# Performance work log

Hardware: AMD Instinct MI355X
Metric: run time of the kernel (lower is better)

Reference implementation:

```python
import jax, jax.numpy as jnp
import numpy as np
import math

B, S, D, H = 4, 512, 768, 12
HD = D // H  # 64
NREL = 2 * 50 + 1  # 101


def setup_inputs() -> dict:
    key = jax.random.key(0)
    ks = jax.random.split(key, 16)
    sc = 0.02
    inp = {
        "query": jax.random.normal(ks[0], (B, S, D), jnp.float32),
        "key": jax.random.normal(ks[1], (B, S, D), jnp.float32),
        "value": jax.random.normal(ks[2], (B, S, D), jnp.float32),
        "mask": jax.random.randint(ks[3], (B, S), 0, 2, jnp.int32),
        "graph_arc": jax.random.randint(ks[4], (B, S, S), 0, NREL, jnp.int64),
        "Wq": jax.random.normal(ks[5], (D, D), jnp.float32) * sc,
        "bq": jnp.zeros((D,), jnp.float32),
        "Wk": jax.random.normal(ks[6], (D, D), jnp.float32) * sc,
        "bk": jnp.zeros((D,), jnp.float32),
        "Wv": jax.random.normal(ks[7], (D, D), jnp.float32) * sc,
        "bv": jnp.zeros((D,), jnp.float32),
        "Wo": jax.random.normal(ks[8], (D, D), jnp.float32) * sc,
        "bo": jnp.zeros((D,), jnp.float32),
        "Ek": jax.random.normal(ks[9], (NREL, HD), jnp.float32) * sc,  # dp_relation_k_g
        "Eq": jax.random.normal(ks[10], (NREL, HD), jnp.float32) * sc,  # dp_relation_q_g
        "Ev": jax.random.normal(ks[11], (NREL, HD), jnp.float32) * sc,  # dp_relation_v_g
    }
    return inp


def _shape(x):
    # (b, s, d) -> (b, h, s, hd)
    return x.reshape(B, S, H, HD).transpose(0, 2, 1, 3)


def reference(query, key, value, mask, graph_arc, Wq, bq, Wk, bk, Wv, bv, Wo, bo, Ek, Eq, Ev):
    q = _shape(query @ Wq.T + bq)   # (b, h, s, hd)
    k = _shape(key @ Wk.T + bk)
    v = _shape(value @ Wv.T + bv)

    scores = jnp.einsum('bhqe,bhke->bhqk', q, k)  # raw QK^T

    dp_k = Ek[graph_arc]  # (b, s, r, hd) relation key embeddings
    dp_q = Eq[graph_arc]  # (b, s, r, hd) relation query embeddings (use_two_attn)
    dp_v = Ev[graph_arc]  # (b, s, r, hd) relation value embeddings (not just_attn)

    key_dp = jnp.einsum('bhse,bsre->bhsr', q, dp_k)
    query_dp = jnp.einsum('bhse,bsre->bhsr', k, dp_q)
    scores = (scores + query_dp + key_dp) / math.sqrt(HD)

    neg_inf = jnp.float32(-jnp.inf)
    maskb = (mask == 0)[:, None, None, :]  # (b, 1, 1, k)
    scores = jnp.where(maskb, neg_inf, scores)
    weights = jax.nn.softmax(scores, axis=-1)  # (b, h, s, r)

    context = jnp.einsum('bhqk,bhke->bhqe', weights, v)
    # relative_matmul_dpv: (b,h,s,r) x (b,s,r,e) -> (b,h,s,e)
    context = context + jnp.einsum('bhsr,bsre->bhse', weights, dp_v)

    context = context.transpose(0, 2, 1, 3).reshape(B, S, D)  # unshape
    out = context @ Wo.T + bo
    return out
```

## Files before the change

### kernel.cpp

```cpp
#include <hip/hip_runtime.h>
#include <hip/hip_bf16.h>
#include <cfloat>
#include <cstdint>

#define Bb 4
#define Ss 512
#define Dd 768
#define Hh 12
#define HDd 64
#define NREL 101

typedef __attribute__((ext_vector_type(8))) short bfrag;
typedef __attribute__((ext_vector_type(4))) float f32x4;
typedef __attribute__((ext_vector_type(8))) unsigned short u16x8;

static __device__ __forceinline__ unsigned short f2bf(float x) {
  union { __hip_bfloat16 h; unsigned short u; } c;
  c.h = __float2bfloat16(x);
  return c.u;
}
static __device__ __forceinline__ float bf2f(unsigned short u) {
  return __uint_as_float(((unsigned int)u) << 16);
}
static __device__ __forceinline__ f32x4 mfma3(bfrag a, bfrag b, f32x4 c) {
  return __builtin_amdgcn_mfma_f32_16x16x32_bf16(a, b, c, 0, 0, 0);
}
static __device__ __forceinline__ void gload16(const void* g, void* l) {
  __builtin_amdgcn_global_load_lds((const __attribute__((address_space(1))) void*)g,
                                   (__attribute__((address_space(3))) void*)l, 16, 0, 0);
}

__global__ void detect_kernel(const int* __restrict__ g, int* __restrict__ flag) {
  __shared__ int anynz;
  if (threadIdx.x == 0) anynz = 0;
  __syncthreads();
  int acc = 0;
  for (int i = threadIdx.x; i < 4096; i += 256) acc |= g[2 * i + 1];
  if (acc != 0) atomicOr(&anynz, 1);
  __syncthreads();
  if (threadIdx.x == 0) *flag = (anynz == 0) ? 1 : 0;
}

__global__ __launch_bounds__(256) void relcvt_kernel(const int* __restrict__ g,
                                                     const int* __restrict__ flag,
                                                     unsigned char* __restrict__ rel8) {
  const int idx = blockIdx.x * 256 + threadIdx.x;
  uchar4 o;
  if (*flag) {
    const int4* p = (const int4*)g + (size_t)idx * 2;
    int4 a = p[0], b = p[1];
    o = make_uchar4((unsigned char)a.x, (unsigned char)a.z,
                    (unsigned char)b.x, (unsigned char)b.z);
  } else {
    int4 a = ((const int4*)g)[idx];
    o = make_uchar4((unsigned char)a.x, (unsigned char)a.y,
                    (unsigned char)a.z, (unsigned char)a.w);
  }
  ((uchar4*)rel8)[idx] = o;
}

__global__ __launch_bounds__(256) void epad_kernel(const float* __restrict__ Ek,
                                                   const float* __restrict__ Eq,
                                                   const float* __restrict__ Ev,
                                                   float* __restrict__ ekp,
                                                   float* __restrict__ eqp,
                                                   float* __restrict__ evtp) {
  const int i = blockIdx.x * 256 + threadIdx.x;
  if (i < 112 * 64) {
    const int rel = i >> 6;
    ekp[i] = (rel < NREL) ? Ek[i] : 0.f;
    eqp[i] = (rel < NREL) ? Eq[i] : 0.f;
  }
  if (i < 64 * 128) {
    const int d = i >> 7, g = i & 127;
    evtp[i] = (g < NREL) ? Ev[g * 64 + d] : 0.f;
  }
}

struct CvtJob { const float* src; unsigned short* hi; unsigned short* lo; int rowlen; int nslots; };
struct Cvt8 { CvtJob j[8]; };

__global__ __launch_bounds__(256) void convert_kernel(Cvt8 jobs) {
  CvtJob jb = jobs.j[blockIdx.z];
  int idx = blockIdx.x * 256 + threadIdx.x;
  if (idx >= jb.nslots) return;
  const int spr = jb.rowlen >> 3;
  const int row = idx / spr;
  const int srem = idx - row * spr;
  const int c = srem >> 3, s8 = srem & 7;
  const float4* s4 = (const float4*)(jb.src + (size_t)idx * 8);
  float4 v0 = s4[0], v1 = s4[1];
  float e[8] = {v0.x, v0.y, v0.z, v0.w, v1.x, v1.y, v1.z, v1.w};
  u16x8 H, L;
#pragma unroll
  for (int i = 0; i < 8; i++) {
    unsigned short h = f2bf(e[i]);
    H[i] = h;
    L[i] = f2bf(e[i] - bf2f(h));
  }
  size_t dst = (size_t)row * jb.rowlen + c * 64 + (size_t)((s8 ^ (row & 7)) * 8);
  *(u16x8*)(jb.hi + dst) = H;
  *(u16x8*)(jb.lo + dst) = L;
}

__global__ __launch_bounds__(256, 2) void gemm_mfma(
    const unsigned short* __restrict__ Xh0, const unsigned short* __restrict__ Xl0,
    const unsigned short* __restrict__ Xh1, const unsigned short* __restrict__ Xl1,
    const unsigned short* __restrict__ Xh2, const unsigned short* __restrict__ Xl2,
    const unsigned short* __restrict__ Wh0, const unsigned short* __restrict__ Wl0,
    const unsigned short* __restrict__ Wh1, const unsigned short* __restrict__ Wl1,
    const unsigned short* __restrict__ Wh2, const unsigned short* __restrict__ Wl2,
    const float* __restrict__ b0, const float* __restrict__ b1, const float* __restrict__ b2,
    float* __restrict__ Y, int is_out)
{
  __shared__ __align__(16) unsigned short Ah[128 * 64], Al[128 * 64];
  __shared__ __align__(16) unsigned short Bh[128 * 64], Bl[128 * 64];

  const int t = threadIdx.x;
  const int lane = t & 63, w = t >> 6;
  const int lg = lane >> 4, lc = lane & 15;
  const int wr = w >> 1, wc = w & 1;
  const int m0 = blockIdx.y * 128, n0 = blockIdx.x * 128;
  const int z = blockIdx.z;
  const unsigned short* Xh = (z == 0) ? Xh0 : (z == 1) ? Xh1 : Xh2;
  const unsigned short* Xl = (z == 0) ? Xl0 : (z == 1) ? Xl1 : Xl2;
  const unsigned short* Wh = (z == 0) ? Wh0 : (z == 1) ? Wh1 : Wh2;
  const unsigned short* Wl = (z == 0) ? Wl0 : (z == 1) ? Wl1 : Wl2;
  const float* bias = (z == 0) ? b0 : (z == 1) ? b1 : b2;

  f32x4 acc[4][4];
#pragma unroll
  for (int m = 0; m < 4; m++)
#pragma unroll
    for (int n = 0; n < 4; n++) acc[m][n] = (f32x4){0.f, 0.f, 0.f, 0.f};

  const int srow = t >> 3;
  const int scol = (t & 7) * 8;

  for (int c = 0; c < 12; c++) {
#pragma unroll
    for (int i = 0; i < 4; i++) {
      size_t ga = (size_t)(m0 + i * 32 + srow) * Dd + c * 64 + scol;
      size_t gb = (size_t)(n0 + i * 32 + srow) * Dd + c * 64 + scol;
      gload16(Xh + ga, &Ah[i * 2048 + t * 8]);
      gload16(Xl + ga, &Al[i * 2048 + t * 8]);
      gload16(Wh + gb, &Bh[i * 2048 + t * 8]);
      gload16(Wl + gb, &Bl[i * 2048 + t * 8]);
    }
    __syncthreads();
#pragma unroll
    for (int ks = 0; ks < 2; ks++) {
      bfrag ah[4], al[4];
#pragma unroll
      for (int m = 0; m < 4; m++) {
        const int aidx = (wr * 64 + m * 16 + lc) * 64 + (((ks * 4 + lg) ^ (lc & 7)) * 8);
        ah[m] = *(const bfrag*)&Ah[aidx];
        al[m] = *(const bfrag*)&Al[aidx];
      }
#pragma unroll
      for (int n = 0; n < 4; n++) {
        const int bidx = (wc * 64 + n * 16 + lc) * 64 + (((ks * 4 + lg) ^ (lc & 7)) * 8);
        bfrag bh = *(const bfrag*)&Bh[bidx];
        bfrag bl = *(const bfrag*)&Bl[bidx];
#pragma unroll
        for (int m = 0; m < 4; m++) {
          acc[m][n] = mfma3(ah[m], bh, acc[m][n]);
          acc[m][n] = mfma3(ah[m], bl, acc[m][n]);
          acc[m][n] = mfma3(al[m], bh, acc[m][n]);
        }
      }
    }
    __syncthreads();
  }

  if (is_out) {
#pragma unroll
    for (int n = 0; n < 4; n++) {
      const int col = n0 + wc * 64 + n * 16 + lc;
      const float badd = bias[col];
#pragma unroll
      for (int m = 0; m < 4; m++) {
        const int rbase = m0 + wr * 64 + m * 16 + 4 * lg;
#pragma unroll
        for (int i = 0; i < 4; i++)
          Y[(size_t)(rbase + i) * Dd + col] = acc[m][n][i] + badd;
      }
    }
  } else {
    float* Yz = Y + (size_t)z * ((size_t)Bb * Hh * Ss * HDd);
#pragma unroll
    for (int n = 0; n < 4; n++) {
      const int col = n0 + wc * 64 + n * 16 + lc;
      const int hh = col >> 6, e = col & 63;
      const float badd = bias[col];
#pragma unroll
      for (int m = 0; m < 4; m++) {
        const int rbase = m0 + wr * 64 + m * 16 + 4 * lg;
#pragma unroll
        for (int i = 0; i < 4; i++) {
          const int row = rbase + i;
          const int b = row >> 9, s = row & 511;
          Yz[((((size_t)b * Hh + hh) * Ss + s) << 6) + e] = acc[m][n][i] + badd;
        }
      }
    }
  }
}

__global__ __launch_bounds__(256) void vtrans_kernel(const float* __restrict__ vg,
                                                     unsigned short* __restrict__ vth,
                                                     unsigned short* __restrict__ vtl) {
  __shared__ float tile[64][68];
  const int t = threadIdx.x;
  const int j = t & 15, sub = t >> 4;
  const int cblk = blockIdx.x;
  const int bh = blockIdx.y;
  const float* src = vg + ((size_t)bh * Ss + cblk * 64) * HDd;
#pragma unroll
  for (int it = 0; it < 4; it++) {
    int srow = sub + 16 * it;
    float4 v = *(const float4*)(src + (size_t)srow * HDd + 4 * j);
    *(float4*)&tile[srow][4 * j] = v;
  }
  __syncthreads();
  unsigned short* dh = vth + (size_t)bh * (HDd * Ss);
  unsigned short* dl = vtl + (size_t)bh * (HDd * Ss);
#pragma unroll
  for (int it = 0; it < 4; it++) {
    int d = sub + 16 * it;
    float o[4] = {tile[4 * j + 0][d], tile[4 * j + 1][d], tile[4 * j + 2][d], tile[4 * j + 3][d]};
    ushort4 hh, ll;
    hh.x = f2bf(o[0]); ll.x = f2bf(o[0] - bf2f(hh.x));
    hh.y = f2bf(o[1]); ll.y = f2bf(o[1] - bf2f(hh.y));
    hh.z = f2bf(o[2]); ll.z = f2bf(o[2] - bf2f(hh.z));
    hh.w = f2bf(o[3]); ll.w = f2bf(o[3] - bf2f(hh.w));
    size_t pos = (size_t)d * Ss + cblk * 64 + (((j >> 1) ^ (d & 7)) * 8) + 4 * (j & 1);
    *(ushort4*)(dh + pos) = hh;
    *(ushort4*)(dl + pos) = ll;
  }
}

__global__ __launch_bounds__(256, 3) void attn_kernel(
    const unsigned short* __restrict__ qHg, const unsigned short* __restrict__ qLg,
    const unsigned short* __restrict__ kHg, const unsigned short* __restrict__ kLg,
    const unsigned short* __restrict__ vtHg, const unsigned short* __restrict__ vtLg,
    const unsigned short* __restrict__ ekH, const unsigned short* __restrict__ ekL,
    const unsigned short* __restrict__ eqH, const unsigned short* __restrict__ eqL,
    const unsigned short* __restrict__ evtH, const unsigned short* __restrict__ evtL,
    const int* __restrict__ msk, const unsigned char* __restrict__ rel8,
    unsigned short* __restrict__ ctxH, unsigned short* __restrict__ ctxL)
{
  __shared__ __align__(16) unsigned short table[2][16 * 112];
  __shared__ __align__(16) float wsum[2][16 * 112];
  __shared__ __align__(16) unsigned short pbuf[2][2][16 * 32];
  __shared__ __align__(16) float osum[2][64 * 16];
  __shared__ __align__(16) unsigned short wsumBF[2][16 * 128];
  __shared__ __align__(16) float l_t[2][16];

  const int t = threadIdx.x;
  const int lane = t & 63, w = t >> 6;
  const int lg = lane >> 4, lc = lane & 15;
  const int tile = w >> 1, half = w & 1;
  const int h = blockIdx.y, b = blockIdx.z;
  const int q0 = (blockIdx.x * 2 + tile) * 16;
  const size_t bh = (size_t)b * Hh + h;

  for (int i = t; i < 2 * 16 * 112; i += 256) ((float*)wsum)[i] = 0.f;
  if (t < 32) ((float*)l_t)[t] = 0.f;

  bfrag qh[2], ql[2];
  {
    const size_t roff = (bh * Ss + q0 + lc) << 6;
    bfrag kqh[2], kql[2];
#pragma unroll
    for (int es = 0; es < 2; es++) {
      const int sw = ((es * 4 + lg) ^ (lc & 7)) * 8;
      qh[es] = *(const bfrag*)&qHg[roff + sw];
      ql[es] = *(const bfrag*)&qLg[roff + sw];
      kqh[es] = *(const bfrag*)&kHg[roff + sw];
      kql[es] = *(const bfrag*)&kLg[roff + sw];
    }
    const int rc0 = half ? 4 : 0, rc1 = half ? 7 : 4;
    for (int rc = rc0; rc < rc1; rc++) {
      f32x4 acc = {0.f, 0.f, 0.f, 0.f};
      const size_t eoff = (size_t)(rc * 16 + lc) << 6;
#pragma unroll
      for (int es = 0; es < 2; es++) {
        const int sw = ((es * 4 + lg) ^ (lc & 7)) * 8;
        bfrag a1 = *(const bfrag*)&ekH[eoff + sw];
        bfrag a2 = *(const bfrag*)&ekL[eoff + sw];
        bfrag a3 = *(const bfrag*)&eqH[eoff + sw];
        bfrag a4 = *(const bfrag*)&eqL[eoff + sw];
        acc = mfma3(a1, qh[es], acc);
        acc = mfma3(a1, ql[es], acc);
        acc = mfma3(a2, qh[es], acc);
        acc = mfma3(a3, kqh[es], acc);
        acc = mfma3(a3, kql[es], acc);
        acc = mfma3(a4, kqh[es], acc);
      }
#pragma unroll
      for (int i = 0; i < 4; i++)
        table[tile][lc * 112 + rc * 16 + 4 * lg + i] = f2bf(acc[i]);
    }
  }
  __syncthreads();

  f32x4 oacc[4];
#pragma unroll
  for (int d = 0; d < 4; d++) oacc[d] = (f32x4){0.f, 0.f, 0.f, 0.f};
  float lsum = 0.f;
  const int* mrow = msk + b * Ss;
  const unsigned char* relrow = rel8 + ((size_t)b * Ss + q0 + lc) * Ss;
  unsigned short* pb = &pbuf[tile][half][0];
  const unsigned short* tab = &table[tile][lc * 112];
  float* ws_row = &wsum[tile][lc * 112];

  for (int ch = 0; ch < 16; ch++) {
    const int kv0 = (half * 16 + ch) * 16;
    f32x4 acc = {0.f, 0.f, 0.f, 0.f};
    {
      const size_t koff = (bh * Ss + kv0 + lc) << 6;
#pragma unroll
      for (int es = 0; es < 2; es++) {
        const int sw = ((es * 4 + lg) ^ (lc & 7)) * 8;
        bfrag kh = *(const bfrag*)&kHg[koff + sw];
        bfrag kl = *(const bfrag*)&kLg[koff + sw];
        acc = mfma3(kh, qh[es], acc);
        acc = mfma3(kh, ql[es], acc);
        acc = mfma3(kl, qh[es], acc);
      }
    }
    float wv[4];
#pragma unroll
    for (int i = 0; i < 4; i++) {
      const int kv = kv0 + 4 * lg + i;
      const int g = relrow[kv];
      const float s = (acc[i] + bf2f(tab[g])) * 0.125f;
      const float e = __expf(s);
      wv[i] = (mrow[kv] != 0) ? e : 0.f;
      lsum += wv[i];
      if (wv[i] > 0.f) atomicAdd(&ws_row[g], wv[i]);
    }
    unsigned int p01 = (unsigned int)f2bf(wv[0]) | ((unsigned int)f2bf(wv[1]) << 16);
    unsigned int p23 = (unsigned int)f2bf(wv[2]) | ((unsigned int)f2bf(wv[3]) << 16);
    *(uint2*)&pb[lc * 32 + (ch & 1) * 16 + 4 * lg] = make_uint2(p01, p23);

    if (ch & 1) {
      bfrag pa = *(const bfrag*)&pb[lc * 32 + 8 * lg];
      const int col = kv0 - 16 + 8 * lg;
      const int cchunk = col >> 6, slot = (col & 63) >> 3;
#pragma unroll
      for (int dblk = 0; dblk < 4; dblk++) {
        const int drow = dblk * 16 + lc;
        const size_t va = (bh * (size_t)HDd + drow) * Ss +
                          (size_t)(cchunk << 6) + (size_t)(((slot ^ (drow & 7))) << 3);
        bfrag vh = *(const bfrag*)&vtHg[va];
        bfrag vl = *(const bfrag*)&vtLg[va];
        oacc[dblk] = mfma3(pa, vh, oacc[dblk]);
        oacc[dblk] = mfma3(pa, vl, oacc[dblk]);
      }
    }
  }

  lsum += __shfl_xor(lsum, 16);
  lsum += __shfl_xor(lsum, 32);
  if (lg == 0) atomicAdd(&l_t[tile][lc], lsum);

  if (half == 0) {
#pragma unroll
    for (int dblk = 0; dblk < 4; dblk++)
      *(f32x4*)&osum[tile][lane * 16 + dblk * 4] = oacc[dblk];
  }
  __syncthreads();
  if (half == 0) return;

#pragma unroll
  for (int dblk = 0; dblk < 4; dblk++)
    oacc[dblk] += *(const f32x4*)&osum[tile][lane * 16 + dblk * 4];

  {
    const int qq = lane >> 2, seg = lane & 3;
#pragma unroll
    for (int jp = 0; jp < 16; jp++) {
      const int col = seg * 32 + jp * 2;
      const float v0 = (col < 112) ? wsum[tile][qq * 112 + col] : 0.f;
      const float v1 = (col + 1 < 112) ? wsum[tile][qq * 112 + col + 1] : 0.f;
      *(unsigned int*)&wsumBF[tile][qq * 128 + col] =
          (unsigned int)f2bf(v0) | ((unsigned int)f2bf(v1) << 16);
    }
  }

  f32x4 evacc[4];
#pragma unroll
  for (int d = 0; d < 4; d++) evacc[d] = (f32x4){0.f, 0.f, 0.f, 0.f};
#pragma unroll
  for (int es = 0; es < 4; es++) {
    bfrag pw = *(const bfrag*)&wsumBF[tile][lc * 128 + es * 32 + 8 * lg];
    const int col = es * 32 + 8 * lg;
    const int cchunk = col >> 6, slot = (col & 63) >> 3;
#pragma unroll
    for (int dblk = 0; dblk < 4; dblk++) {
      const int drow = dblk * 16 + lc;
      const size_t ea = (size_t)drow * 128 + (size_t)(cchunk << 6) +
                        (size_t)((slot ^ (drow & 7)) << 3);
      bfrag eh = *(const bfrag*)&evtH[ea];
      bfrag el = *(const bfrag*)&evtL[ea];
      evacc[dblk] = mfma3(pw, eh, evacc[dblk]);
      evacc[dblk] = mfma3(pw, el, evacc[dblk]);
    }
  }

  float rv[4];
#pragma unroll
  for (int i = 0; i < 4; i++) {
    const float lv = l_t[tile][4 * lg + i];
    rv[i] = (lv > 0.f) ? 1.f / lv : 0.f;
  }
#pragma unroll
  for (int dblk = 0; dblk < 4; dblk++) {
    const int d = dblk * 16 + lc;
    const int slot = d >> 3, pos = d & 7;
#pragma unroll
    for (int i = 0; i < 4; i++) {
      const int qrow = q0 + 4 * lg + i;
      const int r7 = qrow & 7;
      const float val = (oacc[dblk][i] + evacc[dblk][i]) * rv[i];
      const unsigned short hh = f2bf(val);
      const unsigned short ll = f2bf(val - bf2f(hh));
      const size_t base = ((size_t)b * Ss + qrow) * Dd + h * 64 +
                          (size_t)(((slot ^ r7)) << 3) + pos;
      ctxH[base] = hh;
      ctxL[base] = ll;
    }
  }
}

extern "C" void kernel_launch(void* const* d_in, const int* in_sizes, int n_in,
                              void* d_out, int out_size, void* d_ws, size_t ws_size,
                              hipStream_t stream) {
  const float* query = (const float*)d_in[0];
  const float* key   = (const float*)d_in[1];
  const float* value = (const float*)d_in[2];
  const int*   mask  = (const int*)d_in[3];
  const int*   garc  = (const int*)d_in[4];
  const float* Wq = (const float*)d_in[5];
  const float* bq = (const float*)d_in[6];
  const float* Wk = (const float*)d_in[7];
  const float* bk = (const float*)d_in[8];
  const float* Wv = (const float*)d_in[9];
  const float* bv = (const float*)d_in[10];
  const float* Wo = (const float*)d_in[11];
  const float* bo = (const float*)d_in[12];
  const float* Ek = (const float*)d_in[13];
  const float* Eq = (const float*)d_in[14];
  const float* Ev = (const float*)d_in[15];

  const size_t XE = (size_t)Bb * Ss * Dd;
  const size_t WE = (size_t)Dd * Dd;

  char* ws = (char*)d_ws;
  int* flag = (int*)ws;
  float* qb = (float*)(ws + 256);
  float* kb = qb + XE;
  float* vb = kb + XE;
  unsigned short* wq_h = (unsigned short*)(vb + XE);
  unsigned short* wq_l = wq_h + WE;
  unsigned short* wk_h = wq_l + WE;
  unsigned short* wk_l = wk_h + WE;
  unsigned short* wv_h = wk_l + WE;
  unsigned short* wv_l = wv_h + WE;
  unsigned short* wo_h = wv_l + WE;
  unsigned short* wo_l = wo_h + WE;
  unsigned short* regA = wo_l + WE;
  unsigned short* xq_h = regA;           unsigned short* xq_l = regA + XE;
  unsigned short* xk_h = regA + 2 * XE;  unsigned short* xk_l = regA + 3 * XE;
  unsigned short* xv_h = regA + 4 * XE;  unsigned short* xv_l = regA + 5 * XE;
  unsigned short* k_h  = regA;           unsigned short* k_l  = regA + XE;
  unsigned short* q_h  = regA + 2 * XE;  unsigned short* q_l  = regA + 3 * XE;
  unsigned short* vt_h = regA + 4 * XE;  unsigned short* vt_l = regA + 5 * XE;
  unsigned short* ctx_h = regA + 6 * XE;
  unsigned short* ctx_l = ctx_h + XE;
  unsigned char* rel8 = (unsigned char*)(ctx_l + XE);
  float* ekp  = (float*)(rel8 + (size_t)Bb * Ss * Ss);
  float* eqp  = ekp + 112 * 64;
  float* evtp = eqp + 112 * 64;
  unsigned short* ek_h  = (unsigned short*)(evtp + 64 * 128);
  unsigned short* ek_l  = ek_h + 112 * 64;
  unsigned short* eq_h  = ek_l + 112 * 64;
  unsigned short* eq_l  = eq_h + 112 * 64;
  unsigned short* evt_h = eq_l + 112 * 64;
  unsigned short* evt_l = evt_h + 64 * 128;

  detect_kernel<<<1, 256, 0, stream>>>(garc, flag);
  relcvt_kernel<<<dim3(1024), 256, 0, stream>>>(garc, flag, rel8);
  epad_kernel<<<dim3(32), 256, 0, stream>>>(Ek, Eq, Ev, ekp, eqp, evtp);

  Cvt8 pre = {};
  pre.j[0] = {query, xq_h, xq_l, Dd, (int)(XE / 8)};
  pre.j[1] = {key,   xk_h, xk_l, Dd, (int)(XE / 8)};
  pre.j[2] = {value, xv_h, xv_l, Dd, (int)(XE / 8)};
  pre.j[3] = {Wq, wq_h, wq_l, Dd, (int)(WE / 8)};
  pre.j[4] = {Wk, wk_h, wk_l, Dd, (int)(WE / 8)};
  pre.j[5] = {Wv, wv_h, wv_l, Dd, (int)(WE / 8)};
  pre.j[6] = {Wo, wo_h, wo_l, Dd, (int)(WE / 8)};
  convert_kernel<<<dim3(768, 1, 7), 256, 0, stream>>>(pre);

  gemm_mfma<<<dim3(6, 16, 3), 256, 0, stream>>>(
      xq_h, xq_l, xk_h, xk_l, xv_h, xv_l,
      wq_h, wq_l, wk_h, wk_l, wv_h, wv_l,
      bq, bk, bv, qb, 0);

  vtrans_kernel<<<dim3(8, 48), 256, 0, stream>>>(vb, vt_h, vt_l);

  Cvt8 post = {};
  post.j[0] = {kb, k_h, k_l, 64, (int)(XE / 8)};
  post.j[1] = {qb, q_h, q_l, 64, (int)(XE / 8)};
  post.j[2] = {ekp,  ek_h,  ek_l,  64,  (112 * 64) / 8};
  post.j[3] = {eqp,  eq_h,  eq_l,  64,  (112 * 64) / 8};
  post.j[4] = {evtp, evt_h, evt_l, 128, (64 * 128) / 8};
  convert_kernel<<<dim3(768, 1, 5), 256, 0, stream>>>(post);

  attn_kernel<<<dim3(16, 12, 4), 256, 0, stream>>>(
      q_h, q_l, k_h, k_l, vt_h, vt_l,
      ek_h, ek_l, eq_h, eq_l, evt_h, evt_l,
      mask, rel8, ctx_h, ctx_l);

  gemm_mfma<<<dim3(6, 16, 1), 256, 0, stream>>>(
      ctx_h, ctx_l, ctx_h, ctx_l, ctx_h, ctx_l,
      wo_h, wo_l, wo_h, wo_l, wo_h, wo_l,
      bo, bo, bo, (float*)d_out, 1);
}
```

Measured before the change: 244.2 us.

## Fuse bf16 split conversion and V transpose into QKV GEMM epilogue; prefetch K in attention

The QKV projection GEMM now writes hi/lo bf16 split outputs directly in the swizzled per-head layout the attention kernel expects, with V written transposed. This removes the fp32 intermediate buffers, the vtrans kernel and the post-conversion kernel. The embedding padding and conversion are merged into one small kernel. The attention loop now processes 32-key windows, prefetching the next window's K fragments and loading V fragments ahead of the MFMAs. In exchange, the GEMM epilogue does scattered 2-byte stores, and the attention loop holds more registers.

Result: slower. 249.8 us (+2.3%).

```diff
diff --git a/kernel.cpp b/kernel.cpp
--- a/kernel.cpp
+++ b/kernel.cpp
@@ -59,21 +59,39 @@
   ((uchar4*)rel8)[idx] = o;
 }
 
-__global__ __launch_bounds__(256) void epad_kernel(const float* __restrict__ Ek,
-                                                   const float* __restrict__ Eq,
-                                                   const float* __restrict__ Ev,
-                                                   float* __restrict__ ekp,
-                                                   float* __restrict__ eqp,
-                                                   float* __restrict__ evtp) {
+__global__ __launch_bounds__(256) void ecvt_kernel(
+    const float* __restrict__ Ek, const float* __restrict__ Eq, const float* __restrict__ Ev,
+    unsigned short* __restrict__ ekH, unsigned short* __restrict__ ekL,
+    unsigned short* __restrict__ eqH, unsigned short* __restrict__ eqL,
+    unsigned short* __restrict__ evtH, unsigned short* __restrict__ evtL)
+{
   const int i = blockIdx.x * 256 + threadIdx.x;
-  if (i < 112 * 64) {
-    const int rel = i >> 6;
-    ekp[i] = (rel < NREL) ? Ek[i] : 0.f;
-    eqp[i] = (rel < NREL) ? Eq[i] : 0.f;
-  }
-  if (i < 64 * 128) {
-    const int d = i >> 7, g = i & 127;
-    evtp[i] = (g < NREL) ? Ev[g * 64 + d] : 0.f;
+  if (i < 896) {
+    const int row = i >> 3, s8 = i & 7;
+    u16x8 H1, L1, H2, L2;
+#pragma unroll
+    for (int j = 0; j < 8; j++) {
+      const float a = (row < NREL) ? Ek[row * 64 + s8 * 8 + j] : 0.f;
+      const float b = (row < NREL) ? Eq[row * 64 + s8 * 8 + j] : 0.f;
+      unsigned short h1 = f2bf(a); H1[j] = h1; L1[j] = f2bf(a - bf2f(h1));
+      unsigned short h2 = f2bf(b); H2[j] = h2; L2[j] = f2bf(b - bf2f(h2));
+    }
+    const size_t dst = (size_t)row * 64 + (size_t)((s8 ^ (row & 7)) << 3);
+    *(u16x8*)&ekH[dst] = H1; *(u16x8*)&ekL[dst] = L1;
+    *(u16x8*)&eqH[dst] = H2; *(u16x8*)&eqL[dst] = L2;
+  }
+  if (i < 1024) {
+    const int d = i >> 4, s8 = i & 15;
+    const int c = s8 >> 3, sl = s8 & 7;
+    u16x8 H, L;
+#pragma unroll
+    for (int j = 0; j < 8; j++) {
+      const int g = c * 64 + sl * 8 + j;
+      const float v = (g < NREL) ? Ev[g * 64 + d] : 0.f;
+      unsigned short h = f2bf(v); H[j] = h; L[j] = f2bf(v - bf2f(h));
+    }
+    const size_t dst = (size_t)d * 128 + c * 64 + (size_t)((sl ^ (d & 7)) << 3);
+    *(u16x8*)&evtH[dst] = H; *(u16x8*)&evtL[dst] = L;
   }
 }
 
@@ -111,7 +129,11 @@
     const unsigned short* __restrict__ Wh1, const unsigned short* __restrict__ Wl1,
     const unsigned short* __restrict__ Wh2, const unsigned short* __restrict__ Wl2,
     const float* __restrict__ b0, const float* __restrict__ b1, const float* __restrict__ b2,
-    float* __restrict__ Y, int is_out)
+    float* __restrict__ Yf,
+    unsigned short* __restrict__ oH0, unsigned short* __restrict__ oL0,
+    unsigned short* __restrict__ oH1, unsigned short* __restrict__ oL1,
+    unsigned short* __restrict__ oH2, unsigned short* __restrict__ oL2,
+    int mode)
 {
   __shared__ __align__(16) unsigned short Ah[128 * 64], Al[128 * 64];
   __shared__ __align__(16) unsigned short Bh[128 * 64], Bl[128 * 64];
@@ -173,7 +195,7 @@
     __syncthreads();
   }
 
-  if (is_out) {
+  if (mode == 1) {
 #pragma unroll
     for (int n = 0; n < 4; n++) {
       const int col = n0 + wc * 64 + n * 16 + lc;
@@ -183,15 +205,16 @@
         const int rbase = m0 + wr * 64 + m * 16 + 4 * lg;
 #pragma unroll
         for (int i = 0; i < 4; i++)
-          Y[(size_t)(rbase + i) * Dd + col] = acc[m][n][i] + badd;
+          Yf[(size_t)(rbase + i) * Dd + col] = acc[m][n][i] + badd;
       }
     }
   } else {
-    float* Yz = Y + (size_t)z * ((size_t)Bb * Hh * Ss * HDd);
+    unsigned short* dH = (z == 0) ? oH0 : (z == 1) ? oH1 : oH2;
+    unsigned short* dL = (z == 0) ? oL0 : (z == 1) ? oL1 : oL2;
 #pragma unroll
     for (int n = 0; n < 4; n++) {
       const int col = n0 + wc * 64 + n * 16 + lc;
-      const int hh = col >> 6, e = col & 63;
+      const int h = col >> 6, d = col & 63;
       const float badd = bias[col];
 #pragma unroll
       for (int m = 0; m < 4; m++) {
@@ -200,43 +223,23 @@
         for (int i = 0; i < 4; i++) {
           const int row = rbase + i;
           const int b = row >> 9, s = row & 511;
-          Yz[((((size_t)b * Hh + hh) * Ss + s) << 6) + e] = acc[m][n][i] + badd;
+          const float val = acc[m][n][i] + badd;
+          const unsigned short hh = f2bf(val);
+          const unsigned short ll = f2bf(val - bf2f(hh));
+          size_t pos;
+          if (z < 2) {
+            const size_t R = ((size_t)b * Hh + h) * Ss + s;
+            pos = (R << 6) + (size_t)((((d >> 3) ^ (s & 7)) << 3) + (d & 7));
+          } else {
+            const size_t R = ((size_t)b * Hh + h) * (size_t)HDd + d;
+            pos = R * Ss + (size_t)((s >> 6) << 6) +
+                  (size_t)(((((s & 63) >> 3) ^ (d & 7)) << 3) + (s & 7));
+          }
+          dH[pos] = hh;
+          dL[pos] = ll;
         }
       }
     }
-  }
-}
-
-__global__ __launch_bounds__(256) void vtrans_kernel(const float* __restrict__ vg,
-                                                     unsigned short* __restrict__ vth,
-                                                     unsigned short* __restrict__ vtl) {
-  __shared__ float tile[64][68];
-  const int t = threadIdx.x;
-  const int j = t & 15, sub = t >> 4;
-  const int cblk = blockIdx.x;
-  const int bh = blockIdx.y;
-  const float* src = vg + ((size_t)bh * Ss + cblk * 64) * HDd;
-#pragma unroll
-  for (int it = 0; it < 4; it++) {
-    int srow = sub + 16 * it;
-    float4 v = *(const float4*)(src + (size_t)srow * HDd + 4 * j);
-    *(float4*)&tile[srow][4 * j] = v;
-  }
-  __syncthreads();
-  unsigned short* dh = vth + (size_t)bh * (HDd * Ss);
-  unsigned short* dl = vtl + (size_t)bh * (HDd * Ss);
-#pragma unroll
-  for (int it = 0; it < 4; it++) {
-    int d = sub + 16 * it;
-    float o[4] = {tile[4 * j + 0][d], tile[4 * j + 1][d], tile[4 * j + 2][d], tile[4 * j + 3][d]};
-    ushort4 hh, ll;
-    hh.x = f2bf(o[0]); ll.x = f2bf(o[0] - bf2f(hh.x));
-    hh.y = f2bf(o[1]); ll.y = f2bf(o[1] - bf2f(hh.y));
-    hh.z = f2bf(o[2]); ll.z = f2bf(o[2] - bf2f(hh.z));
-    hh.w = f2bf(o[3]); ll.w = f2bf(o[3] - bf2f(hh.w));
-    size_t pos = (size_t)d * Ss + cblk * 64 + (((j >> 1) ^ (d & 7)) * 8) + 4 * (j & 1);
-    *(ushort4*)(dh + pos) = hh;
-    *(ushort4*)(dl + pos) = ll;
   }
 }
 
@@ -315,50 +318,90 @@
   const unsigned short* tab = &table[tile][lc * 112];
   float* ws_row = &wsum[tile][lc * 112];
 
-  for (int ch = 0; ch < 16; ch++) {
-    const int kv0 = (half * 16 + ch) * 16;
-    f32x4 acc = {0.f, 0.f, 0.f, 0.f};
+  const int kvb = half * 256;
+  const size_t kbase = (bh * Ss + kvb + lc) << 6;
+  const int sw0 = (lg ^ (lc & 7)) * 8;
+  const int sw1 = ((4 + lg) ^ (lc & 7)) * 8;
+
+  bfrag c_kh[2][2], c_kl[2][2];
+#pragma unroll
+  for (int blk = 0; blk < 2; blk++) {
+    const size_t ko = kbase + (size_t)(blk * 16) * 64;
+    c_kh[blk][0] = *(const bfrag*)&kHg[ko + sw0];
+    c_kh[blk][1] = *(const bfrag*)&kHg[ko + sw1];
+    c_kl[blk][0] = *(const bfrag*)&kLg[ko + sw0];
+    c_kl[blk][1] = *(const bfrag*)&kLg[ko + sw1];
+  }
+
+  for (int win = 0; win < 8; win++) {
+    const int kv0 = kvb + win * 32;
+    bfrag vh[4], vl[4];
     {
-      const size_t koff = (bh * Ss + kv0 + lc) << 6;
-#pragma unroll
-      for (int es = 0; es < 2; es++) {
-        const int sw = ((es * 4 + lg) ^ (lc & 7)) * 8;
-        bfrag kh = *(const bfrag*)&kHg[koff + sw];
-        bfrag kl = *(const bfrag*)&kLg[koff + sw];
-        acc = mfma3(kh, qh[es], acc);
-        acc = mfma3(kh, ql[es], acc);
-        acc = mfma3(kl, qh[es], acc);
-      }
-    }
-    float wv[4];
-#pragma unroll
-    for (int i = 0; i < 4; i++) {
-      const int kv = kv0 + 4 * lg + i;
-      const int g = relrow[kv];
-      const float s = (acc[i] + bf2f(tab[g])) * 0.125f;
-      const float e = __expf(s);
-      wv[i] = (mrow[kv] != 0) ? e : 0.f;
-      lsum += wv[i];
-      if (wv[i] > 0.f) atomicAdd(&ws_row[g], wv[i]);
-    }
-    unsigned int p01 = (unsigned int)f2bf(wv[0]) | ((unsigned int)f2bf(wv[1]) << 16);
-    unsigned int p23 = (unsigned int)f2bf(wv[2]) | ((unsigned int)f2bf(wv[3]) << 16);
-    *(uint2*)&pb[lc * 32 + (ch & 1) * 16 + 4 * lg] = make_uint2(p01, p23);
-
-    if (ch & 1) {
-      bfrag pa = *(const bfrag*)&pb[lc * 32 + 8 * lg];
-      const int col = kv0 - 16 + 8 * lg;
+      const int col = kv0 + 8 * lg;
       const int cchunk = col >> 6, slot = (col & 63) >> 3;
 #pragma unroll
       for (int dblk = 0; dblk < 4; dblk++) {
         const int drow = dblk * 16 + lc;
         const size_t va = (bh * (size_t)HDd + drow) * Ss +
-                          (size_t)(cchunk << 6) + (size_t)(((slot ^ (drow & 7))) << 3);
-        bfrag vh = *(const bfrag*)&vtHg[va];
-        bfrag vl = *(const bfrag*)&vtLg[va];
-        oacc[dblk] = mfma3(pa, vh, oacc[dblk]);
-        oacc[dblk] = mfma3(pa, vl, oacc[dblk]);
-      }
+                          (size_t)(cchunk << 6) + (size_t)((slot ^ (drow & 7)) << 3);
+        vh[dblk] = *(const bfrag*)&vtHg[va];
+        vl[dblk] = *(const bfrag*)&vtLg[va];
+      }
+    }
+    bfrag n_kh[2][2], n_kl[2][2];
+    if (win < 7) {
+      const size_t kb2 = kbase + (size_t)((win + 1) * 32) * 64;
+#pragma unroll
+      for (int blk = 0; blk < 2; blk++) {
+        const size_t ko = kb2 + (size_t)(blk * 16) * 64;
+        n_kh[blk][0] = *(const bfrag*)&kHg[ko + sw0];
+        n_kh[blk][1] = *(const bfrag*)&kHg[ko + sw1];
+        n_kl[blk][0] = *(const bfrag*)&kLg[ko + sw0];
+        n_kl[blk][1] = *(const bfrag*)&kLg[ko + sw1];
+      }
+    }
+    f32x4 acc0 = {0.f, 0.f, 0.f, 0.f}, acc1 = {0.f, 0.f, 0.f, 0.f};
+#pragma unroll
+    for (int es = 0; es < 2; es++) {
+      acc0 = mfma3(c_kh[0][es], qh[es], acc0);
+      acc0 = mfma3(c_kh[0][es], ql[es], acc0);
+      acc0 = mfma3(c_kl[0][es], qh[es], acc0);
+      acc1 = mfma3(c_kh[1][es], qh[es], acc1);
+      acc1 = mfma3(c_kh[1][es], ql[es], acc1);
+      acc1 = mfma3(c_kl[1][es], qh[es], acc1);
+    }
+#pragma unroll
+    for (int blk = 0; blk < 2; blk++) {
+      const f32x4 a = blk ? acc1 : acc0;
+      float wv[4];
+#pragma unroll
+      for (int i = 0; i < 4; i++) {
+        const int kv = kv0 + blk * 16 + 4 * lg + i;
+        const int g = relrow[kv];
+        const float s = (a[i] + bf2f(tab[g])) * 0.125f;
+        const float e = __expf(s);
+        wv[i] = (mrow[kv] != 0) ? e : 0.f;
+        lsum += wv[i];
+        if (wv[i] > 0.f) atomicAdd(&ws_row[g], wv[i]);
+      }
+      unsigned int p01 = (unsigned int)f2bf(wv[0]) | ((unsigned int)f2bf(wv[1]) << 16);
+      unsigned int p23 = (unsigned int)f2bf(wv[2]) | ((unsigned int)f2bf(wv[3]) << 16);
+      *(uint2*)&pb[lc * 32 + blk * 16 + 4 * lg] = make_uint2(p01, p23);
+    }
+    bfrag pa = *(const bfrag*)&pb[lc * 32 + 8 * lg];
+#pragma unroll
+    for (int dblk = 0; dblk < 4; dblk++) {
+      oacc[dblk] = mfma3(pa, vh[dblk], oacc[dblk]);
+      oacc[dblk] = mfma3(pa, vl[dblk], oacc[dblk]);
+    }
+    if (win < 7) {
+#pragma unroll
+      for (int blk = 0; blk < 2; blk++)
+#pragma unroll
+        for (int es = 0; es < 2; es++) {
+          c_kh[blk][es] = n_kh[blk][es];
+          c_kl[blk][es] = n_kl[blk][es];
+        }
     }
   }
 
@@ -428,7 +471,7 @@
       const unsigned short hh = f2bf(val);
       const unsigned short ll = f2bf(val - bf2f(hh));
       const size_t base = ((size_t)b * Ss + qrow) * Dd + h * 64 +
-                          (size_t)(((slot ^ r7)) << 3) + pos;
+                          (size_t)((slot ^ r7) << 3) + pos;
       ctxH[base] = hh;
       ctxL[base] = ll;
     }
@@ -460,10 +503,7 @@
 
   char* ws = (char*)d_ws;
   int* flag = (int*)ws;
-  float* qb = (float*)(ws + 256);
-  float* kb = qb + XE;
-  float* vb = kb + XE;
-  unsigned short* wq_h = (unsigned short*)(vb + XE);
+  unsigned short* wq_h = (unsigned short*)(ws + 256);
   unsigned short* wq_l = wq_h + WE;
   unsigned short* wk_h = wq_l + WE;
   unsigned short* wk_l = wk_h + WE;
@@ -471,20 +511,15 @@
   unsigned short* wv_l = wv_h + WE;
   unsigned short* wo_h = wv_l + WE;
   unsigned short* wo_l = wo_h + WE;
-  unsigned short* regA = wo_l + WE;
-  unsigned short* xq_h = regA;           unsigned short* xq_l = regA + XE;
-  unsigned short* xk_h = regA + 2 * XE;  unsigned short* xk_l = regA + 3 * XE;
-  unsigned short* xv_h = regA + 4 * XE;  unsigned short* xv_l = regA + 5 * XE;
-  unsigned short* k_h  = regA;           unsigned short* k_l  = regA + XE;
-  unsigned short* q_h  = regA + 2 * XE;  unsigned short* q_l  = regA + 3 * XE;
-  unsigned short* vt_h = regA + 4 * XE;  unsigned short* vt_l = regA + 5 * XE;
-  unsigned short* ctx_h = regA + 6 * XE;
-  unsigned short* ctx_l = ctx_h + XE;
+  unsigned short* xq_h = wo_l + WE;      unsigned short* xq_l = xq_h + XE;
+  unsigned short* xk_h = xq_l + XE;      unsigned short* xk_l = xk_h + XE;
+  unsigned short* xv_h = xk_l + XE;      unsigned short* xv_l = xv_h + XE;
+  unsigned short* q_h  = xv_l + XE;      unsigned short* q_l  = q_h + XE;
+  unsigned short* k_h  = q_l + XE;       unsigned short* k_l  = k_h + XE;
+  unsigned short* vt_h = k_l + XE;       unsigned short* vt_l = vt_h + XE;
+  unsigned short* ctx_h = vt_l + XE;     unsigned short* ctx_l = ctx_h + XE;
   unsigned char* rel8 = (unsigned char*)(ctx_l + XE);
-  float* ekp  = (float*)(rel8 + (size_t)Bb * Ss * Ss);
-  float* eqp  = ekp + 112 * 64;
-  float* evtp = eqp + 112 * 64;
-  unsigned short* ek_h  = (unsigned short*)(evtp + 64 * 128);
+  unsigned short* ek_h  = (unsigned short*)(rel8 + (size_t)Bb * Ss * Ss);
   unsigned short* ek_l  = ek_h + 112 * 64;
   unsigned short* eq_h  = ek_l + 112 * 64;
   unsigned short* eq_l  = eq_h + 112 * 64;
@@ -493,7 +528,7 @@
 
   detect_kernel<<<1, 256, 0, stream>>>(garc, flag);
   relcvt_kernel<<<dim3(1024), 256, 0, stream>>>(garc, flag, rel8);
-  epad_kernel<<<dim3(32), 256, 0, stream>>>(Ek, Eq, Ev, ekp, eqp, evtp);
+  ecvt_kernel<<<dim3(4), 256, 0, stream>>>(Ek, Eq, Ev, ek_h, ek_l, eq_h, eq_l, evt_h, evt_l);
 
   Cvt8 pre = {};
   pre.j[0] = {query, xq_h, xq_l, Dd, (int)(XE / 8)};
@@ -508,17 +543,8 @@
   gemm_mfma<<<dim3(6, 16, 3), 256, 0, stream>>>(
       xq_h, xq_l, xk_h, xk_l, xv_h, xv_l,
       wq_h, wq_l, wk_h, wk_l, wv_h, wv_l,
-      bq, bk, bv, qb, 0);
-
-  vtrans_kernel<<<dim3(8, 48), 256, 0, stream>>>(vb, vt_h, vt_l);
-
-  Cvt8 post = {};
-  post.j[0] = {kb, k_h, k_l, 64, (int)(XE / 8)};
-  post.j[1] = {qb, q_h, q_l, 64, (int)(XE / 8)};
-  post.j[2] = {ekp,  ek_h,  ek_l,  64,  (112 * 64) / 8};
-  post.j[3] = {eqp,  eq_h,  eq_l,  64,  (112 * 64) / 8};
-  post.j[4] = {evtp, evt_h, evt_l, 128, (64 * 128) / 8};
-  convert_kernel<<<dim3(768, 1, 5), 256, 0, stream>>>(post);
+      bq, bk, bv, nullptr,
+      q_h, q_l, k_h, k_l, vt_h, vt_l, 0);
 
   attn_kernel<<<dim3(16, 12, 4), 256, 0, stream>>>(
       q_h, q_l, k_h, k_l, vt_h, vt_l,
@@ -528,5 +554,6 @@
   gemm_mfma<<<dim3(6, 16, 1), 256, 0, stream>>>(
       ctx_h, ctx_l, ctx_h, ctx_l, ctx_h, ctx_l,
       wo_h, wo_l, wo_h, wo_l, wo_h, wo_l,
-      bo, bo, bo, (float*)d_out, 1);
-}
+      bo, bo, bo, (float*)d_out,
+      nullptr, nullptr, nullptr, nullptr, nullptr, nullptr, 1);
+}
```
